# Kernel optimization log

Measured on AMD Instinct MI355X. Metric: run time of the kernel, lower is better.

Reference implementation:

```python
import jax, jax.numpy as jnp
import numpy as np

E, DEPTH, H, T_BLOCK, VOC = 1024, 8, 16, 2048, 256
DH = E // H
B, T = 4, 2048
EPS = 1e-5


def _layernorm(x, g, b):
    mu = jnp.mean(x, axis=-1, keepdims=True)
    var = jnp.mean(jnp.square(x - mu), axis=-1, keepdims=True)
    return (x - mu) * jax.lax.rsqrt(var + EPS) * g + b


def setup_inputs() -> dict:
    key = jax.random.key(0)
    ks = iter(jax.random.split(key, 32))

    def xav(k, shape):
        fan_in, fan_out = shape[-2], shape[-1]
        lim = np.sqrt(6.0 / (fan_in + fan_out))
        return jax.random.uniform(k, shape, jnp.float32, -lim, lim)

    inp = {
        "tokens": jax.random.randint(next(ks), (B, T), 0, VOC),
        "emb_w": xav(next(ks), (VOC, E)),
        "pos_w": xav(next(ks), (T_BLOCK, E)),
        # per-layer stacked params
        "Wq": xav(next(ks), (DEPTH, H, E, DH)),
        "Wk": xav(next(ks), (DEPTH, H, E, DH)),
        "Wv": xav(next(ks), (DEPTH, H, E, DH)),
        "Wo": xav(next(ks), (DEPTH, E, E)),        # stored [in, out]
        "ln1_g": jnp.ones((DEPTH, E)), "ln1_b": jnp.zeros((DEPTH, E)),
        "W1": xav(next(ks), (DEPTH, E, 4 * E)), "b1": jnp.zeros((DEPTH, 4 * E)),
        "W2": xav(next(ks), (DEPTH, 4 * E, E)), "b2": jnp.zeros((DEPTH, E)),
        "ln2_g": jnp.ones((DEPTH, E)), "ln2_b": jnp.zeros((DEPTH, E)),
        "lnf_g": jnp.ones((E,)), "lnf_b": jnp.zeros((E,)),
        "Wu": xav(next(ks), (E, 2)), "bu": jnp.zeros((2,)),
    }
    return inp


def _forward(tokens, emb_w, pos_w, Wq, Wk, Wv, Wo, ln1_g, ln1_b,
             W1, b1, W2, b2, ln2_g, ln2_b, lnf_g, lnf_b, Wu, bu):
    Tlen = tokens.shape[1]
    x = emb_w[tokens] + pos_w[:Tlen]                       # [B, T, E]
    scale = 1.0 / jnp.sqrt(jnp.float32(Tlen))              # NOTE: original divides by sqrt(seq_len)
    for l in range(Wq.shape[0]):
        h = _layernorm(x, ln1_g[l], ln1_b[l])
        q = jnp.einsum('hed,bte->bhtd', Wq[l], h)
        k = jnp.einsum('hed,bte->bhtd', Wk[l], h)
        v = jnp.einsum('hed,bte->bhtd', Wv[l], h)
        scores = jnp.einsum('bhtd,bhsd->bhts', q, k) * scale
        attn = jax.nn.softmax(scores, axis=-1)
        att = jnp.einsum('bhts,bhsd->bhtd', attn, v)       # [B, H, T, DH]
        att = att.transpose(0, 2, 1, 3).reshape(x.shape)   # b t (h d)
        x = x + att @ Wo[l]
        h = _layernorm(x, ln2_g[l], ln2_b[l])
        x = x + jax.nn.relu(h @ W1[l] + b1[l]) @ W2[l] + b2[l]
    x = _layernorm(x, lnf_g, lnf_b)
    return x @ Wu + bu                                     # [B, T, 2]


def reference(tokens, emb_w, pos_w, Wq, Wk, Wv, Wo, ln1_g, ln1_b,
              W1, b1, W2, b2, ln2_g, ln2_b, lnf_g, lnf_b, Wu, bu):
    return _forward(tokens, emb_w, pos_w, Wq, Wk, Wv, Wo, ln1_g, ln1_b,
                    W1, b1, W2, b2, ln2_g, ln2_b, lnf_g, lnf_b, Wu, bu)
```

## Files before the change

kernel.cpp:

```cpp
#include <hip/hip_runtime.h>
#include <hip/hip_bf16.h>
#include <math.h>

#define E_DIM 1024
#define T_SEQ 2048
#define NH 16
#define DHEAD 64
#define NB 4
#define NLAYER 8

typedef __attribute__((ext_vector_type(8))) short bf16x8;
typedef __attribute__((ext_vector_type(4))) short short4v;
typedef __attribute__((ext_vector_type(4))) float f32x4;

#if __has_builtin(__builtin_amdgcn_exp2f)
#define EXP2(x) __builtin_amdgcn_exp2f(x)
#else
#define EXP2(x) exp2f(x)
#endif

static __device__ __forceinline__ short f2bf(float f) {
  union { __hip_bfloat16 h; short s; } u;
  u.h = __float2bfloat16(f);
  return u.s;
}
static __device__ __forceinline__ float bf2f(short s) {
  union { unsigned u; float f; } v;
  v.u = ((unsigned)(unsigned short)s) << 16;
  return v.f;
}

static __device__ __forceinline__ void gload16(const short* g, short* l) {
  __builtin_amdgcn_global_load_lds(
      (const __attribute__((address_space(1))) unsigned*)(g),
      (__attribute__((address_space(3))) unsigned*)(l), 16, 0, 0);
}

static __device__ __forceinline__ int xcd_swz(int orig, int nwg) {
  return (orig & 7) * (nwg >> 3) + (orig >> 3);
}

__global__ __launch_bounds__(256) void embed_kernel(const int* __restrict__ tokens,
    const float* __restrict__ emb, const float* __restrict__ pos, float* __restrict__ x) {
  int idx = blockIdx.x * 256 + threadIdx.x;
  int bt = idx >> 10;
  int e  = idx & 1023;
  int t  = bt & (T_SEQ - 1);
  int tok = tokens[bt];
  x[idx] = emb[tok * E_DIM + e] + pos[t * E_DIM + e];
}

__global__ __launch_bounds__(256) void ln_bf16_kernel(const float* __restrict__ x,
    const float* __restrict__ g, const float* __restrict__ b, short* __restrict__ out) {
  __shared__ float s1[4], s2[4];
  int row = blockIdx.x;
  const float4* xr = (const float4*)(x + (size_t)row * E_DIM);
  float4 xv = xr[threadIdx.x];
  float s = xv.x + xv.y + xv.z + xv.w;
  float q = xv.x*xv.x + xv.y*xv.y + xv.z*xv.z + xv.w*xv.w;
  #pragma unroll
  for (int off = 32; off; off >>= 1) {
    s += __shfl_xor(s, off, 64);
    q += __shfl_xor(q, off, 64);
  }
  int lane = threadIdx.x & 63, wid = threadIdx.x >> 6;
  if (lane == 0) { s1[wid] = s; s2[wid] = q; }
  __syncthreads();
  float mean = (s1[0] + s1[1] + s1[2] + s1[3]) * (1.0f / E_DIM);
  float ms   = (s2[0] + s2[1] + s2[2] + s2[3]) * (1.0f / E_DIM);
  float rstd = rsqrtf(ms - mean * mean + 1e-5f);
  float4 gv = ((const float4*)g)[threadIdx.x];
  float4 bv = ((const float4*)b)[threadIdx.x];
  short4v ov;
  ov.x = f2bf((xv.x - mean) * rstd * gv.x + bv.x);
  ov.y = f2bf((xv.y - mean) * rstd * gv.y + bv.y);
  ov.z = f2bf((xv.z - mean) * rstd * gv.z + bv.z);
  ov.w = f2bf((xv.w - mean) * rstd * gv.w + bv.w);
  *(short4v*)(out + (size_t)row * E_DIM + threadIdx.x * 4) = ov;
}

struct PrepP {
  const float *s0, *s1, *s2, *s3, *s4, *s5;
  short *d0, *d1, *d2, *d3, *d4, *d5;
};

__global__ void prep_kernel(PrepP p) {
  __shared__ float tile[32][33];
  int bid = blockIdx.x;
  const float* src; short* dst; int K, N, kb, local;
  if (bid < 1024)      { src = p.s0; dst = p.d0; K = 1024; N = 64;   kb = 32;  local = bid; }
  else if (bid < 2048) { src = p.s1; dst = p.d1; K = 1024; N = 64;   kb = 32;  local = bid - 1024; }
  else if (bid < 3072) { src = p.s2; dst = p.d2; K = 1024; N = 64;   kb = 32;  local = bid - 2048; }
  else if (bid < 4096) { src = p.s3; dst = p.d3; K = 1024; N = 1024; kb = 32;  local = bid - 3072; }
  else if (bid < 8192) { src = p.s4; dst = p.d4; K = 1024; N = 4096; kb = 32;  local = bid - 4096; }
  else                 { src = p.s5; dst = p.d5; K = 4096; N = 1024; kb = 128; local = bid - 8192; }
  int per = kb * (N >> 5);
  int z = local / per, rem = local % per;
  int k0 = (rem % kb) * 32, n0 = (rem / kb) * 32;
  src += (size_t)z * K * N;
  dst += (size_t)z * N * K;
  int tx = threadIdx.x, ty = threadIdx.y;
  #pragma unroll
  for (int i = 0; i < 4; ++i)
    tile[ty + 8 * i][tx] = src[(size_t)(k0 + ty + 8 * i) * N + n0 + tx];
  __syncthreads();
  #pragma unroll
  for (int i = 0; i < 4; ++i)
    dst[(size_t)(n0 + ty + 8 * i) * K + k0 + tx] = f2bf(tile[tx][ty + 8 * i]);
}

struct GemmP {
  const short* A; const short* B; void* C;
  const float* bias; const float* res;
  long sAb, sAt, sAh;
  long sBh, sBd;
  long sCb, sCt, sCh;
  int K; float alpha; int alphaN; int gridx;
  int relu; int cbf16; int hasbias; int hasres;
};

__global__ __launch_bounds__(512, 1) void gemm_bf16(GemmP p) {
  extern __shared__ __align__(16) short Lsh[];
  constexpr int ASZ  = 128 * 64;
  constexpr int SLOT = ASZ + 256 * 64;

  const int t = threadIdx.x;
  const int lane = t & 63, wid = t >> 6;
  const int wm = wid >> 2, wn = wid & 3;
  const int rA = lane & 15, g = lane >> 4;
  const int wg = xcd_swz(blockIdx.x, gridDim.x);
  const long bm = (long)(wg / p.gridx) * 128, bn = (long)(wg % p.gridx) * 256;

  const int srow8 = lane >> 3;
  const int schunk = (lane & 7) ^ srow8;
  const short* aS[2]; const short* bS[4];
  #pragma unroll
  for (int i = 0; i < 2; ++i) {
    long m = bm + i * 64 + wid * 8 + srow8;
    aS[i] = p.A + (m >> 11) * p.sAb + (m & 2047) * p.sAt + schunk * 8;
  }
  #pragma unroll
  for (int i = 0; i < 4; ++i) {
    long n = bn + i * 64 + wid * 8 + srow8;
    bS[i] = p.B + (n >> 6) * p.sBh + (n & 63) * p.sBd + schunk * 8;
  }
  const int dOff = wid * 512;

#define ISSUE_TILE(slot)                                                      \
  {                                                                           \
    short* sb = Lsh + (slot) * SLOT;                                          \
    _Pragma("unroll")                                                         \
    for (int i = 0; i < 2; ++i) { gload16(aS[i], sb + i * 4096 + dOff); aS[i] += p.sAh; } \
    _Pragma("unroll")                                                         \
    for (int i = 0; i < 4; ++i) { gload16(bS[i], sb + ASZ + i * 4096 + dOff); bS[i] += 64; } \
  }

  f32x4 acc[4][4] = {};
  const int NT = p.K >> 6;

  ISSUE_TILE(0)
  ISSUE_TILE(1)
  asm volatile("s_waitcnt vmcnt(6)" ::: "memory");
  __builtin_amdgcn_s_barrier();

  int rd = 0;
  for (int kt = 0; kt < NT; ++kt) {
    const int wr2 = rd + 2 >= 3 ? rd - 1 : rd + 2;
    if (kt + 2 < NT) ISSUE_TILE(wr2)
    const short* sb = Lsh + rd * SLOT;
    bf16x8 af[4][2], bf[4][2];
    #pragma unroll
    for (int kk = 0; kk < 2; ++kk) {
      const int ch = ((g + kk * 4) ^ (rA & 7)) * 8;
      #pragma unroll
      for (int f = 0; f < 4; ++f) {
        af[f][kk] = *(const bf16x8*)&sb[(wm * 64 + f * 16 + rA) * 64 + ch];
        bf[f][kk] = *(const bf16x8*)&sb[ASZ + (wn * 64 + f * 16 + rA) * 64 + ch];
      }
    }
    asm volatile("s_waitcnt lgkmcnt(0)" ::: "memory");
    __builtin_amdgcn_sched_barrier(0);
    __builtin_amdgcn_s_setprio(1);
    #pragma unroll
    for (int kk = 0; kk < 2; ++kk)
      #pragma unroll
      for (int i = 0; i < 4; ++i)
        #pragma unroll
        for (int j = 0; j < 4; ++j)
          acc[i][j] = __builtin_amdgcn_mfma_f32_16x16x32_bf16(af[i][kk], bf[j][kk], acc[i][j], 0, 0, 0);
    __builtin_amdgcn_s_setprio(0);
    if (kt + 1 < NT) {
      if (kt + 2 < NT) { asm volatile("s_waitcnt vmcnt(6)" ::: "memory"); }
      else             { asm volatile("s_waitcnt vmcnt(0)" ::: "memory"); }
      __builtin_amdgcn_s_barrier();
    }
    rd = rd + 1 >= 3 ? 0 : rd + 1;
  }
#undef ISSUE_TILE

  float bias4[4], aa4[4];
  long ncol[4];
  #pragma unroll
  for (int j = 0; j < 4; ++j) {
    long n = bn + wn * 64 + j * 16 + rA;
    ncol[j] = (n >> 6) * p.sCh + (n & 63);
    bias4[j] = p.hasbias ? p.bias[n] : 0.f;
    aa4[j] = (n < p.alphaN) ? p.alpha : 1.0f;
  }
  #pragma unroll
  for (int i = 0; i < 4; ++i) {
    #pragma unroll
    for (int r = 0; r < 4; ++r) {
      long m = bm + wm * 64 + i * 16 + g * 4 + r;
      long mb = (m >> 11) * p.sCb + (m & 2047) * p.sCt;
      #pragma unroll
      for (int j = 0; j < 4; ++j) {
        long ca = mb + ncol[j];
        float v = aa4[j] * acc[i][j][r] + bias4[j];
        if (p.relu) v = fmaxf(v, 0.f);
        if (p.hasres) v += p.res[ca];
        if (p.cbf16) ((short*)p.C)[ca] = f2bf(v);
        else ((float*)p.C)[ca] = v;
      }
    }
  }
}

__global__ __launch_bounds__(512) void attn_mfma_kernel(const short* __restrict__ qkv,
                                                        short* __restrict__ att) {
  __shared__ __align__(16) short Ks[64 * 64];
  __shared__ __align__(16) short Vt[64 * 64];
  __shared__ __align__(16) short Pq[8 * 16 * 64];

  const int t = threadIdx.x;
  const int lane = t & 63, wid = t >> 6;
  const int wg = xcd_swz(blockIdx.x, gridDim.x);
  const int bh = wg >> 4;
  const int b = bh >> 4, h = bh & 15;
  const int q0blk = (wg & 15) * 128;
  const int rA = lane & 15;
  const int g  = lane >> 4;
  const int xq = (rA & 7) << 3;
  const float L2E = 1.4426950408889634f;

  const short* Qg = qkv + (size_t)b * 6291456 + (size_t)h * 131072;
  const short* Kg = Qg + 2097152;
  const short* Vg = Qg + 4194304;

  const int q0w = q0blk + wid * 16;
  bf16x8 qf0 = *(const bf16x8*)(Qg + (size_t)(q0w + rA) * DHEAD + g * 8);
  bf16x8 qf1 = *(const bf16x8*)(Qg + (size_t)(q0w + rA) * DHEAD + 32 + g * 8);

  bf16x8 ones;
  #pragma unroll
  for (int j = 0; j < 8; ++j) ones[j] = (short)0x3F80;

  short* Pw = Pq + wid * 1024;
  const int ss = t >> 3, sp = t & 7;

  f32x4 lrun4 = {};
  f32x4 acco[4] = {};

  bf16x8 kreg = *(const bf16x8*)(Kg + (size_t)ss * DHEAD + sp * 8);
  bf16x8 vreg = *(const bf16x8*)(Vg + (size_t)ss * DHEAD + sp * 8);

  for (int tile = 0; tile < T_SEQ / 64; ++tile) {
    __syncthreads();
    *(bf16x8*)&Ks[ss * 64 + ((sp ^ (ss & 7)) << 3)] = kreg;
    #pragma unroll
    for (int j = 0; j < 8; ++j) {
      int d = sp * 8 + j;
      Vt[d * 64 + ((ss + 8 * (sp + j)) & 63)] = vreg[j];
    }
    __syncthreads();
    if (tile + 1 < T_SEQ / 64) {
      kreg = *(const bf16x8*)(Kg + (size_t)((tile + 1) * 64 + ss) * DHEAD + sp * 8);
      vreg = *(const bf16x8*)(Vg + (size_t)((tile + 1) * 64 + ss) * DHEAD + sp * 8);
    }

    f32x4 accs[4];
    __builtin_amdgcn_s_setprio(1);
    #pragma unroll
    for (int st = 0; st < 4; ++st) {
      int srow = st * 16 + rA;
      bf16x8 kf0 = *(const bf16x8*)&Ks[srow * 64 + ((g ^ (rA & 7)) << 3)];
      bf16x8 kf1 = *(const bf16x8*)&Ks[srow * 64 + (((g + 4) ^ (rA & 7)) << 3)];
      f32x4 z = {};
      z = __builtin_amdgcn_mfma_f32_16x16x32_bf16(kf0, qf0, z, 0, 0, 0);
      accs[st] = __builtin_amdgcn_mfma_f32_16x16x32_bf16(kf1, qf1, z, 0, 0, 0);
    }
    __builtin_amdgcn_s_setprio(0);

    #pragma unroll
    for (int st = 0; st < 4; ++st) {
      short4v pk;
      pk.x = f2bf(EXP2(accs[st][0] * L2E));
      pk.y = f2bf(EXP2(accs[st][1] * L2E));
      pk.z = f2bf(EXP2(accs[st][2] * L2E));
      pk.w = f2bf(EXP2(accs[st][3] * L2E));
      *(short4v*)&Pw[(rA * 64 + st * 16 + g * 4) ^ xq] = pk;
    }
    asm volatile("s_waitcnt lgkmcnt(0)" ::: "memory");

    __builtin_amdgcn_s_setprio(1);
    #pragma unroll
    for (int sk = 0; sk < 2; ++sk) {
      bf16x8 pf = *(const bf16x8*)&Pw[(rA * 64 + sk * 32 + g * 8) ^ xq];
      lrun4 = __builtin_amdgcn_mfma_f32_16x16x32_bf16(pf, ones, lrun4, 0, 0, 0);
      #pragma unroll
      for (int dt = 0; dt < 4; ++dt) {
        int d = dt * 16 + rA;
        bf16x8 vf = *(const bf16x8*)&Vt[d * 64 +
            ((sk * 32 + g * 8 + 8 * (dt * 2 + (rA >> 3) + (rA & 7))) & 63)];
        acco[dt] = __builtin_amdgcn_mfma_f32_16x16x32_bf16(pf, vf, acco[dt], 0, 0, 0);
      }
    }
    __builtin_amdgcn_s_setprio(0);
  }

  float l4[4];
  #pragma unroll
  for (int r = 0; r < 4; ++r) l4[r] = 1.0f / lrun4[r];
  #pragma unroll
  for (int dt = 0; dt < 4; ++dt)
    #pragma unroll
    for (int r = 0; r < 4; ++r)
      att[(size_t)bh * T_SEQ * DHEAD + (size_t)(q0w + g * 4 + r) * DHEAD + dt * 16 + rA] =
          f2bf(acco[dt][r] * l4[r]);
}

__global__ __launch_bounds__(256) void head_kernel(const short* __restrict__ h,
    const float* __restrict__ Wu, const float* __restrict__ bu, float* __restrict__ out) {
  __shared__ float sm[8];
  int row = blockIdx.x;
  const short* hr = h + (size_t)row * E_DIM;
  float a0 = 0.f, a1 = 0.f;
  for (int i = threadIdx.x; i < E_DIM; i += 256) {
    float hv = bf2f(hr[i]);
    a0 = fmaf(hv, Wu[i * 2 + 0], a0);
    a1 = fmaf(hv, Wu[i * 2 + 1], a1);
  }
  #pragma unroll
  for (int off = 32; off; off >>= 1) {
    a0 += __shfl_xor(a0, off, 64);
    a1 += __shfl_xor(a1, off, 64);
  }
  int lane = threadIdx.x & 63, wid = threadIdx.x >> 6;
  if (lane == 0) { sm[wid] = a0; sm[4 + wid] = a1; }
  __syncthreads();
  if (threadIdx.x == 0) {
    out[row * 2 + 0] = sm[0] + sm[1] + sm[2] + sm[3] + bu[0];
    out[row * 2 + 1] = sm[4] + sm[5] + sm[6] + sm[7] + bu[1];
  }
}

static inline void launch_gemm(hipStream_t stream, int N,
    const short* A, long sAb, long sAt, long sAh,
    const short* B, long sBh, long sBd,
    void* C, long sCb, long sCt, long sCh,
    const float* bias, const float* res, int K, float alpha, int alphaN,
    int relu, int cbf16) {
  GemmP p;
  p.A = A; p.B = B; p.C = C; p.bias = bias; p.res = res;
  p.sAb = sAb; p.sAt = sAt; p.sAh = sAh;
  p.sBh = sBh; p.sBd = sBd;
  p.sCb = sCb; p.sCt = sCt; p.sCh = sCh;
  p.K = K; p.alpha = alpha; p.alphaN = alphaN; p.gridx = N / 256;
  p.relu = relu; p.cbf16 = cbf16;
  p.hasbias = bias != nullptr; p.hasres = res != nullptr;
  int nwg = (N / 256) * ((NB * T_SEQ) / 128);
  gemm_bf16<<<nwg, 512, 147456, stream>>>(p);
}

extern "C" void kernel_launch(void* const* d_in, const int* in_sizes, int n_in,
                              void* d_out, int out_size, void* d_ws, size_t ws_size,
                              hipStream_t stream) {
  const int*   tokens = (const int*)d_in[0];
  const float* emb_w  = (const float*)d_in[1];
  const float* pos_w  = (const float*)d_in[2];
  const float* Wq     = (const float*)d_in[3];
  const float* Wk     = (const float*)d_in[4];
  const float* Wv     = (const float*)d_in[5];
  const float* Wo     = (const float*)d_in[6];
  const float* ln1_g  = (const float*)d_in[7];
  const float* ln1_b  = (const float*)d_in[8];
  const float* W1     = (const float*)d_in[9];
  const float* b1     = (const float*)d_in[10];
  const float* W2     = (const float*)d_in[11];
  const float* b2     = (const float*)d_in[12];
  const float* ln2_g  = (const float*)d_in[13];
  const float* ln2_b  = (const float*)d_in[14];
  const float* lnf_g  = (const float*)d_in[15];
  const float* lnf_b  = (const float*)d_in[16];
  const float* Wu     = (const float*)d_in[17];
  const float* bu     = (const float*)d_in[18];
  float* out = (float*)d_out;

  char* ws = (char*)d_ws;
  float* X     = (float*)(ws);
  short* Hb    = (short*)(ws + 33554432);
  short* QKVb  = (short*)(ws + 50331648);
  short* FFH   = (short*)(ws + 100663296);
  short* WqkvT = (short*)(ws + 167772160);
  short* WoT   = (short*)(ws + 174063616);
  short* W1T   = (short*)(ws + 176160768);
  short* W2T   = (short*)(ws + 184549376);

  const float scale = 0.022097086912079608f;

  embed_kernel<<<32768, 256, 0, stream>>>(tokens, emb_w, pos_w, X);

  for (int l = 0; l < NLAYER; ++l) {
    PrepP pp;
    pp.s0 = Wq + (size_t)l * 1048576; pp.d0 = WqkvT;
    pp.s1 = Wk + (size_t)l * 1048576; pp.d1 = WqkvT + 1048576;
    pp.s2 = Wv + (size_t)l * 1048576; pp.d2 = WqkvT + 2097152;
    pp.s3 = Wo + (size_t)l * 1048576; pp.d3 = WoT;
    pp.s4 = W1 + (size_t)l * 4194304; pp.d4 = W1T;
    pp.s5 = W2 + (size_t)l * 4194304; pp.d5 = W2T;
    prep_kernel<<<12288, dim3(32, 8), 0, stream>>>(pp);

    ln_bf16_kernel<<<8192, 256, 0, stream>>>(X, ln1_g + l * 1024, ln1_b + l * 1024, Hb);

    launch_gemm(stream, 3072, Hb, 2097152, 1024, 64, WqkvT, 65536, 1024,
                QKVb, 6291456, 64, 131072, nullptr, nullptr, 1024, scale, 1024, 0, 1);

    attn_mfma_kernel<<<1024, 512, 0, stream>>>(QKVb, Hb);

    launch_gemm(stream, 1024, Hb, 2097152, 64, 131072, WoT, 65536, 1024,
                X, 2097152, 1024, 64, nullptr, X, 1024, 1.0f, 0, 0, 0);

    ln_bf16_kernel<<<8192, 256, 0, stream>>>(X, ln2_g + l * 1024, ln2_b + l * 1024, Hb);

    launch_gemm(stream, 4096, Hb, 2097152, 1024, 64, W1T, 65536, 1024,
                FFH, 8388608, 4096, 64, b1 + (size_t)l * 4096, nullptr, 1024, 1.0f, 0, 1, 1);
    launch_gemm(stream, 1024, FFH, 8388608, 4096, 64, W2T, 262144, 4096,
                X, 2097152, 1024, 64, b2 + (size_t)l * 1024, X, 4096, 1.0f, 0, 0, 0);
  }

  ln_bf16_kernel<<<8192, 256, 0, stream>>>(X, lnf_g, lnf_b, Hb);
  head_kernel<<<8192, 256, 0, stream>>>(Hb, Wu, bu, out);
}
```

Before: 3.117 ms.

## Use 4 waves per GEMM block with 64x128 per-wave tiles and split LDS waits

The GEMM block drops from 8 waves to 4 while keeping the 128x256 block tile, so each wave now computes a 64x128 sub-tile with 32 accumulators and issues twice as many global-to-LDS loads. The MFMA loop is split by k-half, with a partial lgkmcnt wait, so the first half's matrix ops can start while the second half's LDS reads are still in flight. The aim is more register-level reuse of A/B fragments and less LDS read traffic per MFMA. In exchange, register pressure rises and fewer waves are left to hide latency.

```diff
diff --git a/kernel.cpp b/kernel.cpp
--- a/kernel.cpp
+++ b/kernel.cpp
@@ -119,29 +119,29 @@
   int relu; int cbf16; int hasbias; int hasres;
 };
 
-__global__ __launch_bounds__(512, 1) void gemm_bf16(GemmP p) {
+__global__ __launch_bounds__(256, 1) void gemm_bf16(GemmP p) {
   extern __shared__ __align__(16) short Lsh[];
   constexpr int ASZ  = 128 * 64;
   constexpr int SLOT = ASZ + 256 * 64;
 
   const int t = threadIdx.x;
   const int lane = t & 63, wid = t >> 6;
-  const int wm = wid >> 2, wn = wid & 3;
+  const int wm = wid >> 1, wn = wid & 1;
   const int rA = lane & 15, g = lane >> 4;
   const int wg = xcd_swz(blockIdx.x, gridDim.x);
   const long bm = (long)(wg / p.gridx) * 128, bn = (long)(wg % p.gridx) * 256;
 
   const int srow8 = lane >> 3;
   const int schunk = (lane & 7) ^ srow8;
-  const short* aS[2]; const short* bS[4];
-  #pragma unroll
-  for (int i = 0; i < 2; ++i) {
-    long m = bm + i * 64 + wid * 8 + srow8;
+  const short* aS[4]; const short* bS[8];
+  #pragma unroll
+  for (int i = 0; i < 4; ++i) {
+    long m = bm + i * 32 + wid * 8 + srow8;
     aS[i] = p.A + (m >> 11) * p.sAb + (m & 2047) * p.sAt + schunk * 8;
   }
   #pragma unroll
-  for (int i = 0; i < 4; ++i) {
-    long n = bn + i * 64 + wid * 8 + srow8;
+  for (int i = 0; i < 8; ++i) {
+    long n = bn + i * 32 + wid * 8 + srow8;
     bS[i] = p.B + (n >> 6) * p.sBh + (n & 63) * p.sBd + schunk * 8;
   }
   const int dOff = wid * 512;
@@ -150,17 +150,17 @@
   {                                                                           \
     short* sb = Lsh + (slot) * SLOT;                                          \
     _Pragma("unroll")                                                         \
-    for (int i = 0; i < 2; ++i) { gload16(aS[i], sb + i * 4096 + dOff); aS[i] += p.sAh; } \
+    for (int i = 0; i < 4; ++i) { gload16(aS[i], sb + i * 2048 + dOff); aS[i] += p.sAh; } \
     _Pragma("unroll")                                                         \
-    for (int i = 0; i < 4; ++i) { gload16(bS[i], sb + ASZ + i * 4096 + dOff); bS[i] += 64; } \
-  }
-
-  f32x4 acc[4][4] = {};
+    for (int i = 0; i < 8; ++i) { gload16(bS[i], sb + ASZ + i * 2048 + dOff); bS[i] += 64; } \
+  }
+
+  f32x4 acc[4][8] = {};
   const int NT = p.K >> 6;
 
   ISSUE_TILE(0)
   ISSUE_TILE(1)
-  asm volatile("s_waitcnt vmcnt(6)" ::: "memory");
+  asm volatile("s_waitcnt vmcnt(12)" ::: "memory");
   __builtin_amdgcn_s_barrier();
 
   int rd = 0;
@@ -168,29 +168,37 @@
     const int wr2 = rd + 2 >= 3 ? rd - 1 : rd + 2;
     if (kt + 2 < NT) ISSUE_TILE(wr2)
     const short* sb = Lsh + rd * SLOT;
-    bf16x8 af[4][2], bf[4][2];
+    bf16x8 af[4][2], bf[8][2];
     #pragma unroll
     for (int kk = 0; kk < 2; ++kk) {
       const int ch = ((g + kk * 4) ^ (rA & 7)) * 8;
       #pragma unroll
-      for (int f = 0; f < 4; ++f) {
+      for (int f = 0; f < 4; ++f)
         af[f][kk] = *(const bf16x8*)&sb[(wm * 64 + f * 16 + rA) * 64 + ch];
-        bf[f][kk] = *(const bf16x8*)&sb[ASZ + (wn * 64 + f * 16 + rA) * 64 + ch];
-      }
-    }
+      #pragma unroll
+      for (int j = 0; j < 8; ++j)
+        bf[j][kk] = *(const bf16x8*)&sb[ASZ + (wn * 128 + j * 16 + rA) * 64 + ch];
+    }
+    asm volatile("s_waitcnt lgkmcnt(12)" ::: "memory");
+    __builtin_amdgcn_sched_barrier(0);
+    __builtin_amdgcn_s_setprio(1);
+    #pragma unroll
+    for (int f = 0; f < 4; ++f)
+      #pragma unroll
+      for (int j = 0; j < 8; ++j)
+        acc[f][j] = __builtin_amdgcn_mfma_f32_16x16x32_bf16(af[f][0], bf[j][0], acc[f][j], 0, 0, 0);
+    __builtin_amdgcn_s_setprio(0);
     asm volatile("s_waitcnt lgkmcnt(0)" ::: "memory");
     __builtin_amdgcn_sched_barrier(0);
     __builtin_amdgcn_s_setprio(1);
     #pragma unroll
-    for (int kk = 0; kk < 2; ++kk)
-      #pragma unroll
-      for (int i = 0; i < 4; ++i)
-        #pragma unroll
-        for (int j = 0; j < 4; ++j)
-          acc[i][j] = __builtin_amdgcn_mfma_f32_16x16x32_bf16(af[i][kk], bf[j][kk], acc[i][j], 0, 0, 0);
+    for (int f = 0; f < 4; ++f)
+      #pragma unroll
+      for (int j = 0; j < 8; ++j)
+        acc[f][j] = __builtin_amdgcn_mfma_f32_16x16x32_bf16(af[f][1], bf[j][1], acc[f][j], 0, 0, 0);
     __builtin_amdgcn_s_setprio(0);
     if (kt + 1 < NT) {
-      if (kt + 2 < NT) { asm volatile("s_waitcnt vmcnt(6)" ::: "memory"); }
+      if (kt + 2 < NT) { asm volatile("s_waitcnt vmcnt(12)" ::: "memory"); }
       else             { asm volatile("s_waitcnt vmcnt(0)" ::: "memory"); }
       __builtin_amdgcn_s_barrier();
     }
@@ -198,25 +206,25 @@
   }
 #undef ISSUE_TILE
 
-  float bias4[4], aa4[4];
-  long ncol[4];
-  #pragma unroll
-  for (int j = 0; j < 4; ++j) {
-    long n = bn + wn * 64 + j * 16 + rA;
+  float bias8[8], aa8[8];
+  long ncol[8];
+  #pragma unroll
+  for (int j = 0; j < 8; ++j) {
+    long n = bn + wn * 128 + j * 16 + rA;
     ncol[j] = (n >> 6) * p.sCh + (n & 63);
-    bias4[j] = p.hasbias ? p.bias[n] : 0.f;
-    aa4[j] = (n < p.alphaN) ? p.alpha : 1.0f;
-  }
-  #pragma unroll
-  for (int i = 0; i < 4; ++i) {
+    bias8[j] = p.hasbias ? p.bias[n] : 0.f;
+    aa8[j] = (n < p.alphaN) ? p.alpha : 1.0f;
+  }
+  #pragma unroll
+  for (int f = 0; f < 4; ++f) {
     #pragma unroll
     for (int r = 0; r < 4; ++r) {
-      long m = bm + wm * 64 + i * 16 + g * 4 + r;
+      long m = bm + wm * 64 + f * 16 + g * 4 + r;
       long mb = (m >> 11) * p.sCb + (m & 2047) * p.sCt;
       #pragma unroll
-      for (int j = 0; j < 4; ++j) {
+      for (int j = 0; j < 8; ++j) {
         long ca = mb + ncol[j];
-        float v = aa4[j] * acc[i][j][r] + bias4[j];
+        float v = aa8[j] * acc[f][j][r] + bias8[j];
         if (p.relu) v = fmaxf(v, 0.f);
         if (p.hasres) v += p.res[ca];
         if (p.cbf16) ((short*)p.C)[ca] = f2bf(v);
@@ -369,7 +377,7 @@
   p.relu = relu; p.cbf16 = cbf16;
   p.hasbias = bias != nullptr; p.hasres = res != nullptr;
   int nwg = (N / 256) * ((NB * T_SEQ) / 128);
-  gemm_bf16<<<nwg, 512, 147456, stream>>>(p);
+  gemm_bf16<<<nwg, 256, 147456, stream>>>(p);
 }
 
 extern "C" void kernel_launch(void* const* d_in, const int* in_sizes, int n_in,
```

After: 3.726 ms. 1.2x slower.

## Process two query tiles per wave in attention to reuse K/V LDS tiles

Applied to the files above, without the earlier changes.

Each attention workgroup now covers 256 query rows instead of 128: every wave handles two 16-row query blocks (A and B) against the same staged K and V tiles, and the grid shrinks from 1024 to 512 blocks. This halves the global K/V loads and LDS staging per query row and gives each wave twice as many independent MFMAs between barriers. In exchange, register use rises (two sets of accumulators and Q fragments), the P scratch in LDS doubles, and with half as many workgroups the GPU may be less fully occupied.

```diff
diff --git a/kernel.cpp b/kernel.cpp
--- a/kernel.cpp
+++ b/kernel.cpp
@@ -230,14 +230,14 @@
                                                         short* __restrict__ att) {
   __shared__ __align__(16) short Ks[64 * 64];
   __shared__ __align__(16) short Vt[64 * 64];
-  __shared__ __align__(16) short Pq[8 * 16 * 64];
+  __shared__ __align__(16) short Pq[8 * 2048];
 
   const int t = threadIdx.x;
   const int lane = t & 63, wid = t >> 6;
   const int wg = xcd_swz(blockIdx.x, gridDim.x);
-  const int bh = wg >> 4;
+  const int bh = wg >> 3;
   const int b = bh >> 4, h = bh & 15;
-  const int q0blk = (wg & 15) * 128;
+  const int q0blk = (wg & 7) * 256;
   const int rA = lane & 15;
   const int g  = lane >> 4;
   const int xq = (rA & 7) << 3;
@@ -247,19 +247,23 @@
   const short* Kg = Qg + 2097152;
   const short* Vg = Qg + 4194304;
 
-  const int q0w = q0blk + wid * 16;
-  bf16x8 qf0 = *(const bf16x8*)(Qg + (size_t)(q0w + rA) * DHEAD + g * 8);
-  bf16x8 qf1 = *(const bf16x8*)(Qg + (size_t)(q0w + rA) * DHEAD + 32 + g * 8);
+  const int qA = q0blk + wid * 16;
+  const int qB = qA + 128;
+  bf16x8 qfA0 = *(const bf16x8*)(Qg + (size_t)(qA + rA) * DHEAD + g * 8);
+  bf16x8 qfA1 = *(const bf16x8*)(Qg + (size_t)(qA + rA) * DHEAD + 32 + g * 8);
+  bf16x8 qfB0 = *(const bf16x8*)(Qg + (size_t)(qB + rA) * DHEAD + g * 8);
+  bf16x8 qfB1 = *(const bf16x8*)(Qg + (size_t)(qB + rA) * DHEAD + 32 + g * 8);
 
   bf16x8 ones;
   #pragma unroll
   for (int j = 0; j < 8; ++j) ones[j] = (short)0x3F80;
 
-  short* Pw = Pq + wid * 1024;
+  short* PwA = Pq + wid * 2048;
+  short* PwB = PwA + 1024;
   const int ss = t >> 3, sp = t & 7;
 
-  f32x4 lrun4 = {};
-  f32x4 acco[4] = {};
+  f32x4 lrunA = {}, lrunB = {};
+  f32x4 accoA[4] = {}, accoB[4] = {};
 
   bf16x8 kreg = *(const bf16x8*)(Kg + (size_t)ss * DHEAD + sp * 8);
   bf16x8 vreg = *(const bf16x8*)(Vg + (size_t)ss * DHEAD + sp * 8);
@@ -278,55 +282,68 @@
       vreg = *(const bf16x8*)(Vg + (size_t)((tile + 1) * 64 + ss) * DHEAD + sp * 8);
     }
 
-    f32x4 accs[4];
+    f32x4 accsA[4], accsB[4];
     __builtin_amdgcn_s_setprio(1);
     #pragma unroll
     for (int st = 0; st < 4; ++st) {
       int srow = st * 16 + rA;
       bf16x8 kf0 = *(const bf16x8*)&Ks[srow * 64 + ((g ^ (rA & 7)) << 3)];
       bf16x8 kf1 = *(const bf16x8*)&Ks[srow * 64 + (((g + 4) ^ (rA & 7)) << 3)];
-      f32x4 z = {};
-      z = __builtin_amdgcn_mfma_f32_16x16x32_bf16(kf0, qf0, z, 0, 0, 0);
-      accs[st] = __builtin_amdgcn_mfma_f32_16x16x32_bf16(kf1, qf1, z, 0, 0, 0);
+      f32x4 zA = {}, zB = {};
+      zA = __builtin_amdgcn_mfma_f32_16x16x32_bf16(kf0, qfA0, zA, 0, 0, 0);
+      zB = __builtin_amdgcn_mfma_f32_16x16x32_bf16(kf0, qfB0, zB, 0, 0, 0);
+      accsA[st] = __builtin_amdgcn_mfma_f32_16x16x32_bf16(kf1, qfA1, zA, 0, 0, 0);
+      accsB[st] = __builtin_amdgcn_mfma_f32_16x16x32_bf16(kf1, qfB1, zB, 0, 0, 0);
     }
     __builtin_amdgcn_s_setprio(0);
 
     #pragma unroll
     for (int st = 0; st < 4; ++st) {
-      short4v pk;
-      pk.x = f2bf(EXP2(accs[st][0] * L2E));
-      pk.y = f2bf(EXP2(accs[st][1] * L2E));
-      pk.z = f2bf(EXP2(accs[st][2] * L2E));
-      pk.w = f2bf(EXP2(accs[st][3] * L2E));
-      *(short4v*)&Pw[(rA * 64 + st * 16 + g * 4) ^ xq] = pk;
+      short4v pkA;
+      pkA.x = f2bf(EXP2(accsA[st][0] * L2E));
+      pkA.y = f2bf(EXP2(accsA[st][1] * L2E));
+      pkA.z = f2bf(EXP2(accsA[st][2] * L2E));
+      pkA.w = f2bf(EXP2(accsA[st][3] * L2E));
+      *(short4v*)&PwA[(rA * 64 + st * 16 + g * 4) ^ xq] = pkA;
+      short4v pkB;
+      pkB.x = f2bf(EXP2(accsB[st][0] * L2E));
+      pkB.y = f2bf(EXP2(accsB[st][1] * L2E));
+      pkB.z = f2bf(EXP2(accsB[st][2] * L2E));
+      pkB.w = f2bf(EXP2(accsB[st][3] * L2E));
+      *(short4v*)&PwB[(rA * 64 + st * 16 + g * 4) ^ xq] = pkB;
     }
     asm volatile("s_waitcnt lgkmcnt(0)" ::: "memory");
 
     __builtin_amdgcn_s_setprio(1);
     #pragma unroll
     for (int sk = 0; sk < 2; ++sk) {
-      bf16x8 pf = *(const bf16x8*)&Pw[(rA * 64 + sk * 32 + g * 8) ^ xq];
-      lrun4 = __builtin_amdgcn_mfma_f32_16x16x32_bf16(pf, ones, lrun4, 0, 0, 0);
+      bf16x8 pfA = *(const bf16x8*)&PwA[(rA * 64 + sk * 32 + g * 8) ^ xq];
+      bf16x8 pfB = *(const bf16x8*)&PwB[(rA * 64 + sk * 32 + g * 8) ^ xq];
+      lrunA = __builtin_amdgcn_mfma_f32_16x16x32_bf16(pfA, ones, lrunA, 0, 0, 0);
+      lrunB = __builtin_amdgcn_mfma_f32_16x16x32_bf16(pfB, ones, lrunB, 0, 0, 0);
       #pragma unroll
       for (int dt = 0; dt < 4; ++dt) {
         int d = dt * 16 + rA;
         bf16x8 vf = *(const bf16x8*)&Vt[d * 64 +
             ((sk * 32 + g * 8 + 8 * (dt * 2 + (rA >> 3) + (rA & 7))) & 63)];
-        acco[dt] = __builtin_amdgcn_mfma_f32_16x16x32_bf16(pf, vf, acco[dt], 0, 0, 0);
+        accoA[dt] = __builtin_amdgcn_mfma_f32_16x16x32_bf16(pfA, vf, accoA[dt], 0, 0, 0);
+        accoB[dt] = __builtin_amdgcn_mfma_f32_16x16x32_bf16(pfB, vf, accoB[dt], 0, 0, 0);
       }
     }
     __builtin_amdgcn_s_setprio(0);
   }
 
-  float l4[4];
-  #pragma unroll
-  for (int r = 0; r < 4; ++r) l4[r] = 1.0f / lrun4[r];
+  float lA[4], lB[4];
+  #pragma unroll
+  for (int r = 0; r < 4; ++r) { lA[r] = 1.0f / lrunA[r]; lB[r] = 1.0f / lrunB[r]; }
+  const size_t obase = (size_t)bh * T_SEQ * DHEAD;
   #pragma unroll
   for (int dt = 0; dt < 4; ++dt)
     #pragma unroll
-    for (int r = 0; r < 4; ++r)
-      att[(size_t)bh * T_SEQ * DHEAD + (size_t)(q0w + g * 4 + r) * DHEAD + dt * 16 + rA] =
-          f2bf(acco[dt][r] * l4[r]);
+    for (int r = 0; r < 4; ++r) {
+      att[obase + (size_t)(qA + g * 4 + r) * DHEAD + dt * 16 + rA] = f2bf(accoA[dt][r] * lA[r]);
+      att[obase + (size_t)(qB + g * 4 + r) * DHEAD + dt * 16 + rA] = f2bf(accoB[dt][r] * lB[r]);
+    }
 }
 
 __global__ __launch_bounds__(256) void head_kernel(const short* __restrict__ h,
@@ -425,7 +442,7 @@
     launch_gemm(stream, 3072, Hb, 2097152, 1024, 64, WqkvT, 65536, 1024,
                 QKVb, 6291456, 64, 131072, nullptr, nullptr, 1024, scale, 1024, 0, 1);
 
-    attn_mfma_kernel<<<1024, 512, 0, stream>>>(QKVb, Hb);
+    attn_mfma_kernel<<<512, 512, 0, stream>>>(QKVb, Hb);
 
     launch_gemm(stream, 1024, Hb, 2097152, 64, 131072, WoT, 65536, 1024,
                 X, 2097152, 1024, 64, nullptr, X, 1024, 1.0f, 0, 0, 0);
```

Result: faster. 3.046 ms (-2.3%).
